# Kernel optimization log

Hardware: AMD Instinct MI355X
Metric: run time of the kernel (lower is better)

## Reference

```python
import jax, jax.numpy as jnp
import numpy as np

IN_CH, H0, H1, OUT_CH = 6, 128, 256, 256
EPS = 1e-5

def _layernorm(x, g, b):
    mu = jnp.mean(x, axis=-1, keepdims=True)
    var = jnp.mean(jnp.square(x - mu), axis=-1, keepdims=True)
    return (x - mu) * jax.lax.rsqrt(var + EPS) * g + b

def setup_inputs() -> dict:
    key = jax.random.key(0)
    ks = jax.random.split(key, 12)
    B, N, C = 8, 65536, 1024
    inp = {
        "point_patches": jax.random.normal(ks[0], (B, N, IN_CH), jnp.float32),
        "nn_idx": jax.random.randint(ks[1], (B, N), 0, C, jnp.int64),
        "center_number": C,
        # conv1: Linear(6,128) -> LN(128) -> GELU -> Linear(128,128)
        "w1": jax.random.normal(ks[2], (IN_CH, H0), jnp.float32) / np.sqrt(IN_CH),
        "b1": jnp.zeros((H0,), jnp.float32),
        "g1": jnp.ones((H0,), jnp.float32),
        "beta1": jnp.zeros((H0,), jnp.float32),
        "w2": jax.random.normal(ks[3], (H0, H0), jnp.float32) / np.sqrt(H0),
        "b2": jnp.zeros((H0,), jnp.float32),
        # conv2: Linear(256,256) -> LN(256) -> GELU -> Linear(256,256)
        "w3": jax.random.normal(ks[4], (2 * H0, H1), jnp.float32) / np.sqrt(2 * H0),
        "b3": jnp.zeros((H1,), jnp.float32),
        "g2": jnp.ones((H1,), jnp.float32),
        "beta2": jnp.zeros((H1,), jnp.float32),
        "w4": jax.random.normal(ks[5], (H1, OUT_CH), jnp.float32) / np.sqrt(H1),
        "b4": jnp.zeros((OUT_CH,), jnp.float32),
    }
    return inp

def _scatter_max_zeros(x, nn_idx, center_number):
    # torch.scatter_reduce(zeros, 1, idx, x, 'max') with include_self=True:
    # segment max clamped from below at 0; empty centers stay 0.
    B = x.shape[0]
    y = jnp.zeros((B, center_number, x.shape[-1]), x.dtype)
    return y.at[jnp.arange(B)[:, None], nn_idx].max(x)

def reference(point_patches, nn_idx, center_number, w1, b1, g1, beta1, w2, b2, w3, b3, g2, beta2, w4, b4):
    # conv1 MLP
    h = point_patches @ w1 + b1
    h = jax.nn.gelu(_layernorm(h, g1, beta1), approximate=False)
    x = h @ w2 + b2                                   # [B, N, H0]
    # scatter-max to centers, gather back per point
    y = _scatter_max_zeros(x, nn_idx, center_number)  # [B, C, H0]
    x_max = jnp.take_along_axis(y, nn_idx[:, :, None], axis=1)  # [B, N, H0]
    x = jnp.concatenate([x_max, x], axis=-1)          # [B, N, 2*H0]
    # conv2 MLP
    h = x @ w3 + b3
    h = jax.nn.gelu(_layernorm(h, g2, beta2), approximate=False)
    x = h @ w4 + b4                                   # [B, N, OUT]
    return _scatter_max_zeros(x, nn_idx, center_number)  # [B, C, OUT]
```

## Files before the change

kernel.cpp:

```cpp
#include <hip/hip_runtime.h>

typedef short short8 __attribute__((ext_vector_type(8)));
typedef float f32x4 __attribute__((ext_vector_type(4)));

#define DEVI __device__ __forceinline__

constexpr int BATCH = 8;
constexpr int NPTS  = 65536;
constexpr int CIN   = 6;
constexpr int H0    = 128;
constexpr int H1    = 256;
constexpr int NCTR  = 1024;
constexpr int MB    = 64;
constexpr int NCHUNK = 8;
constexpr int CHSZ  = NPTS / NCHUNK;

constexpr int A1S = 136;
constexpr int A2S = 264;

constexpr int CAP1 = 8;
constexpr int CAP2 = 4;

constexpr size_t Y_BYTES  = (size_t)BATCH * NCTR * H0 * 4;
constexpr size_t W2T_OFF  = Y_BYTES;
constexpr size_t W3T_OFF  = W2T_OFF + (size_t)H0 * H0 * 2;
constexpr size_t W4T_OFF  = W3T_OFF + (size_t)H1 * H1 * 2;
constexpr size_t SORT_OFF = W4T_OFF + (size_t)H1 * H1 * 2;
constexpr size_t CH_OFF   = SORT_OFF + (size_t)BATCH * NPTS * 4;
constexpr size_t CB_OFF   = CH_OFF + (size_t)BATCH * NCHUNK * NCTR * 4;
constexpr size_t NZR_OFF  = CB_OFF + (size_t)BATCH * NCHUNK * NCTR * 4;
constexpr size_t YQ_OFF   = NZR_OFF + (size_t)BATCH * NCTR * 4;
constexpr size_t WS_NEED  = YQ_OFF + (size_t)BATCH * NCTR * H0 * 2;
constexpr size_t XQ_OFF   = WS_NEED;
constexpr size_t WS_XQ    = XQ_OFF + (size_t)BATCH * NPTS * H0 * 2;

DEVI unsigned short f2bf(float f) {
    unsigned u = __float_as_uint(f);
    u += 0x7fffu + ((u >> 16) & 1u);
    return (unsigned short)(u >> 16);
}
DEVI float gelu(float x) {
    const float x3 = x * x * x;
    const float u = fmaf(x3, -0.07135481283f, -1.5957691216f * x);
    return x * __builtin_amdgcn_rcpf(1.f + __expf(u));
}

DEVI void conv1_tile(int tid, const float* s_pts, const float* s_w1,
                     const float* s_b1, const float* s_g1, const float* s_be1,
                     unsigned short* a1)
{
    const int p = tid >> 2, sub = tid & 3;
    float pt[CIN];
#pragma unroll
    for (int k = 0; k < CIN; ++k) pt[k] = s_pts[p * CIN + k];
    float h[32];
#pragma unroll
    for (int j = 0; j < 32; ++j) {
        const int c = (j << 2) + sub;
        float a = s_b1[c];
#pragma unroll
        for (int k = 0; k < CIN; ++k) a = fmaf(pt[k], s_w1[k * H0 + c], a);
        h[j] = a;
    }
    float s = 0.f, s2 = 0.f;
#pragma unroll
    for (int j = 0; j < 32; ++j) { s += h[j]; s2 = fmaf(h[j], h[j], s2); }
    s  += __shfl_xor(s, 1);  s  += __shfl_xor(s, 2);
    s2 += __shfl_xor(s2, 1); s2 += __shfl_xor(s2, 2);
    const float mean = s * (1.f / H0);
    const float rstd = rsqrtf(s2 * (1.f / H0) - mean * mean + 1e-5f);
#pragma unroll
    for (int j = 0; j < 32; ++j) {
        const int c = (j << 2) + sub;
        float v = fmaf((h[j] - mean) * rstd, s_g1[c], s_be1[c]);
        a1[p * A1S + c] = f2bf(gelu(v));
    }
}

DEVI void gemm2(int lane, int wave, const unsigned short* a1,
                const unsigned short* __restrict__ w2T, f32x4 (&acc)[4][2])
{
    const int q = lane >> 4, colw = lane & 15, n0 = wave * 32;
#pragma unroll
    for (int ks = 0; ks < 4; ++ks) {
        short8 af[4], bfr[2];
#pragma unroll
        for (int mt = 0; mt < 4; ++mt)
            af[mt] = *(const short8*)&a1[(mt * 16 + colw) * A1S + ks * 32 + q * 8];
#pragma unroll
        for (int nt = 0; nt < 2; ++nt)
            bfr[nt] = *(const short8*)&w2T[(n0 + nt * 16 + colw) * H0 + ks * 32 + q * 8];
#pragma unroll
        for (int mt = 0; mt < 4; ++mt)
#pragma unroll
            for (int nt = 0; nt < 2; ++nt)
                acc[mt][nt] = __builtin_amdgcn_mfma_f32_16x16x32_bf16(
                    af[mt], bfr[nt], acc[mt][nt], 0, 0, 0);
    }
}

DEVI void stage_sorted(int tid, int b, int P0, const int* __restrict__ sorted,
                       const float* __restrict__ pts, float* s_pts, int* s_idx)
{
    if (tid < 64) {
        const int val = sorted[P0 + tid];
        const int pid = val & 0xFFFF;
        s_idx[tid] = (val >> 16) & (NCTR - 1);
        const float* prow = &pts[((size_t)(b << 16) + pid) * CIN];
#pragma unroll
        for (int k = 0; k < CIN; ++k) s_pts[tid * CIN + k] = prow[k];
    }
}

DEVI void slot_scan(int tid, const int* s_idx, int* s_slot, int* s_slotc, int* s_nslot, int cap)
{
    int f = 0;
    if (tid < MB) {
        f = (tid > 0 && s_idx[tid] != s_idx[tid - 1]) ? 1 : 0;
        s_slot[tid] = f;
    }
    __syncthreads();
#pragma unroll
    for (int off = 1; off < MB; off <<= 1) {
        int t = 0;
        if (tid < MB && tid >= off) t = s_slot[tid - off];
        __syncthreads();
        if (tid < MB) s_slot[tid] += t;
        __syncthreads();
    }
    if (tid < MB) {
        const int s = s_slot[tid];
        if ((f || tid == 0) && s < cap) s_slotc[s] = s_idx[tid];
        if (tid == MB - 1) *s_nslot = (s + 1 < cap) ? (s + 1) : cap;
    }
    __syncthreads();
}

__global__ __launch_bounds__(256) void k_prep(
    const float* __restrict__ w2, const float* __restrict__ w3,
    const float* __restrict__ w4,
    unsigned short* __restrict__ w2T, unsigned short* __restrict__ w3T,
    unsigned short* __restrict__ w4T)
{
    int t = blockIdx.x * 256 + threadIdx.x;
    if (t < H0 * H0) {
        int n = t >> 7, k = t & 127;
        w2T[t] = f2bf(w2[k * H0 + n]);
    }
    int t3 = t - H0 * H0;
    if (t3 >= 0 && t3 < H1 * H1) {
        int n = t3 >> 8, k = t3 & 255;
        w3T[t3] = f2bf(w3[k * H1 + n]);
    }
    int t4 = t - (H0 * H0 + H1 * H1);
    if (t4 >= 0 && t4 < H1 * H1) {
        int n = t4 >> 8, k = t4 & 255;
        w4T[t4] = f2bf(w4[k * H1 + n]);
    }
}

__global__ __launch_bounds__(256) void k_yq(const float* __restrict__ y,
                                            unsigned short* __restrict__ yq)
{
    const int i = blockIdx.x * 256 + threadIdx.x;
    const float4 v = *(const float4*)&y[(size_t)i * 4];
    uint2 pk;
    pk.x = (unsigned)f2bf(v.x) | ((unsigned)f2bf(v.y) << 16);
    pk.y = (unsigned)f2bf(v.z) | ((unsigned)f2bf(v.w) << 16);
    *(uint2*)&yq[(size_t)i * 4] = pk;
}

__global__ __launch_bounds__(256) void k_hist(const int* __restrict__ nn,
                                              int* __restrict__ ch)
{
    __shared__ int lh[NCTR];
    const int tid = threadIdx.x;
    const int b = blockIdx.x >> 3, k = blockIdx.x & 7;
    const int base = (b << 16) + k * CHSZ;
    for (int c = tid; c < NCTR; c += 256) lh[c] = 0;
    __syncthreads();
    for (int i = tid; i < CHSZ; i += 256)
        atomicAdd(&lh[nn[base + i] & (NCTR - 1)], 1);
    __syncthreads();
    for (int c = tid; c < NCTR; c += 256) ch[(blockIdx.x << 10) + c] = lh[c];
}

__global__ __launch_bounds__(256) void k_scan(const int* __restrict__ ch,
                                              int* __restrict__ cb,
                                              int* __restrict__ nzr)
{
    __shared__ int part[256], partz[256];
    const int tid = threadIdx.x;
    const int b = tid >> 5, t = tid & 31;
    const int c0 = t * 32;
    int tot = 0, totz = 0;
    for (int c = c0; c < c0 + 32; ++c) {
        int cnt = 0;
        for (int k = 0; k < NCHUNK; ++k)
            cnt += ch[((b * NCHUNK + k) << 10) + c];
        tot += cnt; totz += (cnt > 0);
    }
    part[tid] = tot; partz[tid] = totz;
    __syncthreads();
    if (t == 0) {
        int run = 0, runz = 0;
        for (int i = 0; i < 32; ++i) {
            const int v  = part[(b << 5) + i];  part[(b << 5) + i]  = run;  run  += v;
            const int vz = partz[(b << 5) + i]; partz[(b << 5) + i] = runz; runz += vz;
        }
    }
    __syncthreads();
    int run = part[tid], runz = partz[tid];
    for (int c = c0; c < c0 + 32; ++c) {
        int cnt = 0;
        for (int k = 0; k < NCHUNK; ++k) {
            const int idx = ((b * NCHUNK + k) << 10) + c;
            cb[idx] = run; run += ch[idx]; cnt += ch[idx];
        }
        nzr[(b << 10) + c] = runz;
        runz += (cnt > 0);
    }
}

__global__ __launch_bounds__(256) void k_scatter(const int* __restrict__ nn,
                                                 const int* __restrict__ cb,
                                                 int* __restrict__ sorted)
{
    __shared__ int cur[NCTR];
    const int tid = threadIdx.x;
    const int b = blockIdx.x >> 3, k = blockIdx.x & 7;
    const int base = (b << 16) + k * CHSZ;
    for (int c = tid; c < NCTR; c += 256) cur[c] = cb[(blockIdx.x << 10) + c];
    __syncthreads();
    for (int i = tid; i < CHSZ; i += 256) {
        const int c = nn[base + i] & (NCTR - 1);
        const int pos = atomicAdd(&cur[c], 1);
        if ((unsigned)pos < (unsigned)NPTS)
            sorted[(b << 16) + pos] = (k * CHSZ + i) | (c << 16);
    }
}

template <bool XQ>
__global__ __launch_bounds__(256, 4) void k_phase1(
    const int* __restrict__ sorted, const float* __restrict__ pts,
    const int* __restrict__ nzr,
    const float* __restrict__ w1, const float* __restrict__ b1,
    const float* __restrict__ g1, const float* __restrict__ be1,
    const unsigned short* __restrict__ w2T, const float* __restrict__ b2,
    float* __restrict__ y, unsigned short* __restrict__ xq)
{
    __shared__ __align__(16) float s_pts[MB * CIN];
    __shared__ int   s_idx[MB], s_slot[MB], s_slotc[CAP1], s_nslot;
    __shared__ float s_w1[CIN * H0];
    __shared__ float s_b1[H0], s_g1[H0], s_be1[H0];
    __shared__ __align__(16) unsigned short a1[MB * A1S];
    __shared__ int   red1[CAP1 * H0];

    const int tid = threadIdx.x;
    const int P0  = blockIdx.x * MB;
    const int b   = P0 >> 16;
    const int lane = tid & 63, wave = tid >> 6;
    const int q = lane >> 4, colw = lane & 15, n0 = wave * 32;

    if (tid < 64) {
        const int val = sorted[P0 + tid];
        const int pid = val & 0xFFFF;
        const int c   = (val >> 16) & (NCTR - 1);
        const int c0v = (sorted[P0] >> 16) & (NCTR - 1);
        s_idx[tid] = c;
        const int sl = nzr[(b << 10) + c] - nzr[(b << 10) + c0v];
        s_slot[tid] = sl;
        if (tid == 63) s_nslot = (sl + 1 < CAP1) ? (sl + 1) : CAP1;
        const float* prow = &pts[((size_t)(b << 16) + pid) * CIN];
#pragma unroll
        for (int k = 0; k < CIN; ++k) s_pts[tid * CIN + k] = prow[k];
    }
    for (int i = tid; i < CIN * H0; i += 256) s_w1[i] = w1[i];
    if (tid < H0) { s_b1[tid] = b1[tid]; s_g1[tid] = g1[tid]; s_be1[tid] = be1[tid]; }
    for (int i = tid; i < CAP1 * H0; i += 256) red1[i] = 0;
    __syncthreads();

    if (tid < 64) {
        const int sl = s_slot[tid];
        if (sl < CAP1 && (tid == 0 || s_idx[tid] != s_idx[tid - 1]))
            s_slotc[sl] = s_idx[tid];
    }
    conv1_tile(tid, s_pts, s_w1, s_b1, s_g1, s_be1, a1);
    __syncthreads();

    f32x4 acc[4][2] = {};
    gemm2(lane, wave, a1, w2T, acc);
    if (XQ) __syncthreads();

    float b2reg[2];
#pragma unroll
    for (int nt = 0; nt < 2; ++nt) b2reg[nt] = b2[n0 + nt * 16 + colw];

    int* yi = (int*)y;
    {
        float vm[2] = {-3.4e38f, -3.4e38f};
        int cur = s_slot[q * 4], curc = s_idx[q * 4];
#pragma unroll
        for (int mt = 0; mt < 4; ++mt)
#pragma unroll
            for (int r = 0; r < 4; ++r) {
                const int row = mt * 16 + q * 4 + r;
                const int s = s_slot[row];
                if (s != cur) {
#pragma unroll
                    for (int nt = 0; nt < 2; ++nt) {
                        if (vm[nt] > 0.f) {
                            const int col = n0 + nt * 16 + colw;
                            if (cur < CAP1) atomicMax(&red1[cur * H0 + col], __float_as_int(vm[nt]));
                            else atomicMax(&yi[(((b << 10) + curc) << 7) + col], __float_as_int(vm[nt]));
                        }
                        vm[nt] = -3.4e38f;
                    }
                    cur = s; curc = s_idx[row];
                }
#pragma unroll
                for (int nt = 0; nt < 2; ++nt) {
                    const float v = acc[mt][nt][r] + b2reg[nt];
                    if (XQ) a1[row * A1S + n0 + nt * 16 + colw] = f2bf(v);
                    vm[nt] = fmaxf(vm[nt], v);
                }
            }
#pragma unroll
        for (int nt = 0; nt < 2; ++nt)
            if (vm[nt] > 0.f) {
                const int col = n0 + nt * 16 + colw;
                if (cur < CAP1) atomicMax(&red1[cur * H0 + col], __float_as_int(vm[nt]));
                else atomicMax(&yi[(((b << 10) + curc) << 7) + col], __float_as_int(vm[nt]));
            }
    }
    __syncthreads();
    const int nsc = s_nslot;
    for (int i = tid; i < nsc * H0; i += 256) {
        const int v = red1[i];
        if (v > 0)
            atomicMax(&yi[(((b << 10) + s_slotc[i >> 7]) << 7) + (i & 127)], v);
    }
    if (XQ) {
        for (int i = tid; i < MB * (H0 / 8); i += 256) {
            const int row = i >> 4, u = (i & 15) * 8;
            *(short8*)&xq[((size_t)P0 + row) * H0 + u] = *(const short8*)&a1[row * A1S + u];
        }
    }
}

__global__ __launch_bounds__(512, 6) void k_phase2x(
    const int* __restrict__ sorted, const unsigned short* __restrict__ xq,
    const unsigned short* __restrict__ yq, const int* __restrict__ nzr,
    const unsigned short* __restrict__ w3T, const float* __restrict__ b3,
    const float* __restrict__ g2, const float* __restrict__ be2,
    const unsigned short* __restrict__ w4T, const float* __restrict__ b4,
    float* __restrict__ outp)
{
    __shared__ int   s_idx[MB], s_slot[MB], s_slotc[CAP2], s_nslot;
    __shared__ __align__(16) unsigned short a2[MB * A2S];
    __shared__ union __align__(16) {
        float2 stats[MB * 8];
        int    red[CAP2 * H1];
    } u2;
    __shared__ float2 s_rowstat[MB];

    const int tid = threadIdx.x;
    const int P0  = blockIdx.x * MB;
    const int b   = P0 >> 16;
    const int lane = tid & 63, wave = tid >> 6;
    const int q = lane >> 4, colw = lane & 15;
    const int n0 = wave * 32;

    const int rowp = tid >> 3, sub = tid & 7;
    {
        const int sval = sorted[P0 + rowp];
        const int cp = (sval >> 16) & (NCTR - 1);
        const unsigned short* src;
        unsigned short* dst;
        if (sub < 4) {
            src = &yq[((size_t)((b << 10) + cp)) * H0 + sub * 32];
            dst = &a2[rowp * A2S + sub * 32];
        } else {
            src = &xq[((size_t)P0 + rowp) * H0 + (sub - 4) * 32];
            dst = &a2[rowp * A2S + H0 + (sub - 4) * 32];
        }
#pragma unroll
        for (int u = 0; u < 4; ++u)
            *(short8*)(dst + u * 8) = *(const short8*)(src + u * 8);
    }
    if (tid < 64) {
        const int c   = (sorted[P0 + tid] >> 16) & (NCTR - 1);
        const int c0v = (sorted[P0] >> 16) & (NCTR - 1);
        s_idx[tid] = c;
        const int sl = nzr[(b << 10) + c] - nzr[(b << 10) + c0v];
        s_slot[tid] = sl;
        if (tid == 63) s_nslot = (sl + 1 < CAP2) ? (sl + 1) : CAP2;
    }
    __syncthreads();

    if (tid < 64) {
        const int sl = s_slot[tid];
        if (sl < CAP2 && (tid == 0 || s_idx[tid] != s_idx[tid - 1]))
            s_slotc[sl] = s_idx[tid];
    }

    f32x4 acc3[4][2] = {};
#pragma unroll
    for (int ks = 0; ks < 8; ++ks) {
        short8 af[4], bfr[2];
#pragma unroll
        for (int mt = 0; mt < 4; ++mt)
            af[mt] = *(const short8*)&a2[(mt * 16 + colw) * A2S + ks * 32 + q * 8];
#pragma unroll
        for (int nt = 0; nt < 2; ++nt)
            bfr[nt] = *(const short8*)&w3T[(n0 + nt * 16 + colw) * H1 + ks * 32 + q * 8];
#pragma unroll
        for (int mt = 0; mt < 4; ++mt)
#pragma unroll
            for (int nt = 0; nt < 2; ++nt)
                acc3[mt][nt] = __builtin_amdgcn_mfma_f32_16x16x32_bf16(
                    af[mt], bfr[nt], acc3[mt][nt], 0, 0, 0);
    }

    {
        float b3r[2];
#pragma unroll
        for (int nt = 0; nt < 2; ++nt) b3r[nt] = b3[n0 + nt * 16 + colw];
#pragma unroll
        for (int mt = 0; mt < 4; ++mt)
#pragma unroll
            for (int nt = 0; nt < 2; ++nt)
#pragma unroll
                for (int r = 0; r < 4; ++r)
                    acc3[mt][nt][r] += b3r[nt];
    }

#pragma unroll
    for (int mt = 0; mt < 4; ++mt)
#pragma unroll
        for (int r = 0; r < 4; ++r) {
            float s = 0.f, s2 = 0.f;
#pragma unroll
            for (int nt = 0; nt < 2; ++nt) {
                float v = acc3[mt][nt][r];
                s += v; s2 = fmaf(v, v, s2);
            }
            s  += __shfl_xor(s, 1);  s  += __shfl_xor(s, 2);
            s  += __shfl_xor(s, 4);  s  += __shfl_xor(s, 8);
            s2 += __shfl_xor(s2, 1); s2 += __shfl_xor(s2, 2);
            s2 += __shfl_xor(s2, 4); s2 += __shfl_xor(s2, 8);
            if (colw == 0)
                u2.stats[(mt * 16 + q * 4 + r) * 8 + wave] = make_float2(s, s2);
        }
    __syncthreads();
    if (tid < MB) {
        float S = 0.f, S2 = 0.f;
#pragma unroll
        for (int w = 0; w < 8; ++w) { float2 t = u2.stats[tid * 8 + w]; S += t.x; S2 += t.y; }
        const float mean = S * (1.f / H1);
        const float rstd = rsqrtf(S2 * (1.f / H1) - mean * mean + 1e-5f);
        s_rowstat[tid] = make_float2(mean, rstd);
    }
    __syncthreads();

    {
        float g2r[2], be2r[2];
#pragma unroll
        for (int nt = 0; nt < 2; ++nt) {
            const int col = n0 + nt * 16 + colw;
            g2r[nt] = g2[col]; be2r[nt] = be2[col];
        }
#pragma unroll
        for (int mt = 0; mt < 4; ++mt)
#pragma unroll
            for (int r = 0; r < 4; ++r) {
                const int row = mt * 16 + q * 4 + r;
                const float2 ms = s_rowstat[row];
#pragma unroll
                for (int nt = 0; nt < 2; ++nt) {
                    float v = (acc3[mt][nt][r] - ms.x) * ms.y;
                    v = fmaf(v, g2r[nt], be2r[nt]);
                    a2[row * A2S + n0 + nt * 16 + colw] = f2bf(gelu(v));
                }
            }
    }
    for (int i = tid; i < CAP2 * H1; i += 512) u2.red[i] = 0;
    __syncthreads();

    f32x4 acc4[4][2] = {};
#pragma unroll
    for (int ks = 0; ks < 8; ++ks) {
        short8 af[4], bfr[2];
#pragma unroll
        for (int mt = 0; mt < 4; ++mt)
            af[mt] = *(const short8*)&a2[(mt * 16 + colw) * A2S + ks * 32 + q * 8];
#pragma unroll
        for (int nt = 0; nt < 2; ++nt)
            bfr[nt] = *(const short8*)&w4T[(n0 + nt * 16 + colw) * H1 + ks * 32 + q * 8];
#pragma unroll
        for (int mt = 0; mt < 4; ++mt)
#pragma unroll
            for (int nt = 0; nt < 2; ++nt)
                acc4[mt][nt] = __builtin_amdgcn_mfma_f32_16x16x32_bf16(
                    af[mt], bfr[nt], acc4[mt][nt], 0, 0, 0);
    }

    float b4r[2];
#pragma unroll
    for (int nt = 0; nt < 2; ++nt) b4r[nt] = b4[n0 + nt * 16 + colw];

    int* outi = (int*)outp;
    {
        float vm[2] = {-3.4e38f, -3.4e38f};
        int cur = s_slot[q * 4], curc = s_idx[q * 4];
#pragma unroll
        for (int mt = 0; mt < 4; ++mt)
#pragma unroll
            for (int r = 0; r < 4; ++r) {
                const int row = mt * 16 + q * 4 + r;
                const int s = s_slot[row];
                if (s != cur) {
#pragma unroll
                    for (int nt = 0; nt < 2; ++nt) {
                        if (vm[nt] > 0.f) {
                            const int col = n0 + nt * 16 + colw;
                            if (cur < CAP2) atomicMax(&u2.red[cur * H1 + col], __float_as_int(vm[nt]));
                            else atomicMax(&outi[(((size_t)(b << 10) + curc) << 8) + col], __float_as_int(vm[nt]));
                        }
                        vm[nt] = -3.4e38f;
                    }
                    cur = s; curc = s_idx[row];
                }
#pragma unroll
                for (int nt = 0; nt < 2; ++nt)
                    vm[nt] = fmaxf(vm[nt], acc4[mt][nt][r] + b4r[nt]);
            }
#pragma unroll
        for (int nt = 0; nt < 2; ++nt)
            if (vm[nt] > 0.f) {
                const int col = n0 + nt * 16 + colw;
                if (cur < CAP2) atomicMax(&u2.red[cur * H1 + col], __float_as_int(vm[nt]));
                else atomicMax(&outi[(((size_t)(b << 10) + curc) << 8) + col], __float_as_int(vm[nt]));
            }
    }
    __syncthreads();
    const int nsc = s_nslot;
    for (int i = tid; i < nsc * H1; i += 512) {
        const int v = u2.red[i];
        if (v > 0)
            atomicMax(&outi[(((size_t)(b << 10) + s_slotc[i >> 8]) << 8) + (i & 255)], v);
    }
}

__global__ __launch_bounds__(256) void k_phase2r(
    const int* __restrict__ sorted, const float* __restrict__ pts,
    const float* __restrict__ w1, const float* __restrict__ b1,
    const float* __restrict__ g1, const float* __restrict__ be1,
    const unsigned short* __restrict__ w2T, const float* __restrict__ b2,
    const float* __restrict__ y,
    const unsigned short* __restrict__ w3T, const float* __restrict__ b3,
    const float* __restrict__ g2, const float* __restrict__ be2,
    const unsigned short* __restrict__ w4T, const float* __restrict__ b4,
    float* __restrict__ outp)
{
    __shared__ __align__(16) float s_pts[MB * CIN];
    __shared__ int   s_idx[MB], s_slot[MB], s_slotc[CAP2], s_nslot;
    __shared__ float s_w1[CIN * H0];
    __shared__ float s_b1[H0], s_g1[H0], s_be1[H0], s_b2[H0];
    __shared__ float s_b3[H1], s_g2[H1], s_be2[H1], s_b4[H1];
    __shared__ union __align__(16) {
        unsigned short a1[MB * A1S];
        struct { float2 stats[MB * 4]; float2 rowstat[MB]; } ln;
        int red[CAP2 * H1];
    } u1;
    __shared__ __align__(16) unsigned short a2[MB * A2S];

    const int tid = threadIdx.x;
    const int P0  = blockIdx.x * MB;
    const int b   = P0 >> 16;

    stage_sorted(tid, b, P0, sorted, pts, s_pts, s_idx);
    for (int i = tid; i < CIN * H0; i += 256) s_w1[i] = w1[i];
    if (tid < H0) { s_b1[tid] = b1[tid]; s_g1[tid] = g1[tid]; s_be1[tid] = be1[tid]; s_b2[tid] = b2[tid]; }
    if (tid < H1) { s_b3[tid] = b3[tid]; s_g2[tid] = g2[tid]; s_be2[tid] = be2[tid]; s_b4[tid] = b4[tid]; }
    __syncthreads();

    conv1_tile(tid, s_pts, s_w1, s_b1, s_g1, s_be1, u1.a1);
    slot_scan(tid, s_idx, s_slot, s_slotc, &s_nslot, CAP2);

    f32x4 acc2[4][2] = {};
    const int lane = tid & 63, wave = tid >> 6;
    gemm2(lane, wave, u1.a1, w2T, acc2);

    const int q = lane >> 4, colw = lane & 15;
    {
        const int n0 = wave * 32;
#pragma unroll
        for (int mt = 0; mt < 4; ++mt)
#pragma unroll
            for (int nt = 0; nt < 2; ++nt)
#pragma unroll
                for (int r = 0; r < 4; ++r) {
                    const int row = mt * 16 + q * 4 + r;
                    const int col = n0 + nt * 16 + colw;
                    a2[row * A2S + H0 + col] = f2bf(acc2[mt][nt][r] + s_b2[col]);
                }
    }
    {
        const int p = tid >> 2, sub = tid & 3;
        const float* yrow = y + ((size_t)((b << 10) + s_idx[p])) * H0;
#pragma unroll
        for (int j4 = 0; j4 < 8; ++j4) {
            const int c = sub * 32 + j4 * 4;
            float4 v = *(const float4*)&yrow[c];
            uint2 pk;
            pk.x = (unsigned)f2bf(v.x) | ((unsigned)f2bf(v.y) << 16);
            pk.y = (unsigned)f2bf(v.z) | ((unsigned)f2bf(v.w) << 16);
            *(uint2*)&a2[p * A2S + c] = pk;
        }
    }
    __syncthreads();

    f32x4 acc3[4][4] = {};
    const int n0 = wave * 64;
#pragma unroll
    for (int ks = 0; ks < 8; ++ks) {
        short8 af[4], bfr[4];
#pragma unroll
        for (int mt = 0; mt < 4; ++mt)
            af[mt] = *(const short8*)&a2[(mt * 16 + colw) * A2S + ks * 32 + q * 8];
#pragma unroll
        for (int nt = 0; nt < 4; ++nt)
            bfr[nt] = *(const short8*)&w3T[(n0 + nt * 16 + colw) * H1 + ks * 32 + q * 8];
#pragma unroll
        for (int mt = 0; mt < 4; ++mt)
#pragma unroll
            for (int nt = 0; nt < 4; ++nt)
                acc3[mt][nt] = __builtin_amdgcn_mfma_f32_16x16x32_bf16(
                    af[mt], bfr[nt], acc3[mt][nt], 0, 0, 0);
    }

#pragma unroll
    for (int mt = 0; mt < 4; ++mt)
#pragma unroll
        for (int nt = 0; nt < 4; ++nt)
#pragma unroll
            for (int r = 0; r < 4; ++r)
                acc3[mt][nt][r] += s_b3[n0 + nt * 16 + colw];

#pragma unroll
    for (int mt = 0; mt < 4; ++mt)
#pragma unroll
        for (int r = 0; r < 4; ++r) {
            float s = 0.f, s2 = 0.f;
#pragma unroll
            for (int nt = 0; nt < 4; ++nt) {
                float v = acc3[mt][nt][r];
                s += v; s2 = fmaf(v, v, s2);
            }
            s  += __shfl_xor(s, 1);  s  += __shfl_xor(s, 2);
            s  += __shfl_xor(s, 4);  s  += __shfl_xor(s, 8);
            s2 += __shfl_xor(s2, 1); s2 += __shfl_xor(s2, 2);
            s2 += __shfl_xor(s2, 4); s2 += __shfl_xor(s2, 8);
            if (colw == 0)
                u1.ln.stats[(mt * 16 + q * 4 + r) * 4 + wave] = make_float2(s, s2);
        }
    __syncthreads();
    if (tid < MB) {
        float S = 0.f, S2 = 0.f;
#pragma unroll
        for (int w = 0; w < 4; ++w) { float2 t = u1.ln.stats[tid * 4 + w]; S += t.x; S2 += t.y; }
        const float mean = S * (1.f / H1);
        const float rstd = rsqrtf(S2 * (1.f / H1) - mean * mean + 1e-5f);
        u1.ln.rowstat[tid] = make_float2(mean, rstd);
    }
    __syncthreads();

#pragma unroll
    for (int mt = 0; mt < 4; ++mt)
#pragma unroll
        for (int r = 0; r < 4; ++r) {
            const int row = mt * 16 + q * 4 + r;
            const float2 ms = u1.ln.rowstat[row];
#pragma unroll
            for (int nt = 0; nt < 4; ++nt) {
                const int col = n0 + nt * 16 + colw;
                float v = (acc3[mt][nt][r] - ms.x) * ms.y;
                v = fmaf(v, s_g2[col], s_be2[col]);
                a2[row * A2S + col] = f2bf(gelu(v));
            }
        }
    __syncthreads();

    for (int i = tid; i < CAP2 * H1; i += 256) u1.red[i] = 0;

    f32x4 acc4[4][4] = {};
#pragma unroll
    for (int ks = 0; ks < 8; ++ks) {
        short8 af[4], bfr[4];
#pragma unroll
        for (int mt = 0; mt < 4; ++mt)
            af[mt] = *(const short8*)&a2[(mt * 16 + colw) * A2S + ks * 32 + q * 8];
#pragma unroll
        for (int nt = 0; nt < 4; ++nt)
            bfr[nt] = *(const short8*)&w4T[(n0 + nt * 16 + colw) * H1 + ks * 32 + q * 8];
#pragma unroll
        for (int mt = 0; mt < 4; ++mt)
#pragma unroll
            for (int nt = 0; nt < 4; ++nt)
                acc4[mt][nt] = __builtin_amdgcn_mfma_f32_16x16x32_bf16(
                    af[mt], bfr[nt], acc4[mt][nt], 0, 0, 0);
    }
    __syncthreads();

    int* outi = (int*)outp;
#pragma unroll
    for (int mt = 0; mt < 4; ++mt)
#pragma unroll
        for (int nt = 0; nt < 4; ++nt)
#pragma unroll
            for (int r = 0; r < 4; ++r) {
                const int row = mt * 16 + q * 4 + r;
                const int col = n0 + nt * 16 + colw;
                const float v = acc4[mt][nt][r] + s_b4[col];
                if (v > 0.f) {
                    const int s = s_slot[row];
                    if (s < CAP2)
                        atomicMax(&u1.red[s * H1 + col], __float_as_int(v));
                    else
                        atomicMax(&outi[(((size_t)(b << 10) + s_idx[row]) << 8) + col],
                                  __float_as_int(v));
                }
            }
    __syncthreads();
    const int nsc = s_nslot;
    for (int i = tid; i < nsc * H1; i += 256) {
        const int v = u1.red[i];
        if (v > 0)
            atomicMax(&outi[(((size_t)(b << 10) + s_slotc[i >> 8]) << 8) + (i & 255)], v);
    }
}

extern "C" void kernel_launch(void* const* d_in, const int* in_sizes, int n_in,
                              void* d_out, int out_size, void* d_ws, size_t ws_size,
                              hipStream_t stream)
{
    const float* pts = (const float*)d_in[0];
    const int*   nn  = (const int*)d_in[1];
    const float* w1  = (const float*)d_in[3];
    const float* b1  = (const float*)d_in[4];
    const float* g1  = (const float*)d_in[5];
    const float* be1 = (const float*)d_in[6];
    const float* w2  = (const float*)d_in[7];
    const float* b2  = (const float*)d_in[8];
    const float* w3  = (const float*)d_in[9];
    const float* b3  = (const float*)d_in[10];
    const float* g2  = (const float*)d_in[11];
    const float* be2 = (const float*)d_in[12];
    const float* w4  = (const float*)d_in[13];
    const float* b4  = (const float*)d_in[14];

    if (ws_size < WS_NEED) return;

    char* ws = (char*)d_ws;
    float*          y      = (float*)(ws);
    unsigned short* w2T    = (unsigned short*)(ws + W2T_OFF);
    unsigned short* w3T    = (unsigned short*)(ws + W3T_OFF);
    unsigned short* w4T    = (unsigned short*)(ws + W4T_OFF);
    int*            sorted = (int*)(ws + SORT_OFF);
    int*            ch     = (int*)(ws + CH_OFF);
    int*            cb     = (int*)(ws + CB_OFF);
    int*            nzr    = (int*)(ws + NZR_OFF);
    unsigned short* yq     = (unsigned short*)(ws + YQ_OFF);
    unsigned short* xq     = (unsigned short*)(ws + XQ_OFF);
    float* outp = (float*)d_out;
    const bool have_xq = ws_size >= WS_XQ;

    hipMemsetAsync(y, 0, Y_BYTES, stream);
    hipMemsetAsync(outp, 0, (size_t)out_size * sizeof(float), stream);

    k_prep<<<576, 256, 0, stream>>>(w2, w3, w4, w2T, w3T, w4T);
    k_hist<<<BATCH * NCHUNK, 256, 0, stream>>>(nn, ch);
    k_scan<<<1, 256, 0, stream>>>(ch, cb, nzr);
    k_scatter<<<BATCH * NCHUNK, 256, 0, stream>>>(nn, cb, sorted);

    const int nblk = BATCH * NPTS / MB;
    if (have_xq) {
        k_phase1<true><<<nblk, 256, 0, stream>>>(sorted, pts, nzr, w1, b1, g1, be1, w2T, b2, y, xq);
        k_yq<<<BATCH * NCTR * H0 / 4 / 256, 256, 0, stream>>>(y, yq);
        k_phase2x<<<nblk, 512, 0, stream>>>(sorted, xq, yq, nzr, w3T, b3, g2, be2, w4T, b4, outp);
    } else {
        k_phase1<false><<<nblk, 256, 0, stream>>>(sorted, pts, nzr, w1, b1, g1, be1, w2T, b2, y, nullptr);
        k_phase2r<<<nblk, 256, 0, stream>>>(sorted, pts, w1, b1, g1, be1, w2T, b2, y,
                                            w3T, b3, g2, be2, w4T, b4, outp);
    }
}
```

Measured before the change: 441.6 us.

## Make phase2x persistent over four tiles with register prefetch of next tile

The phase-2 kernel now processes four 64-point tiles per block in a grid-strided loop, launching a quarter as many blocks. While the current tile is computed, it loads the next tile's gathered yq/xq rows into registers so global latency overlaps with MFMA work. This amortizes block launch and prologue cost, at the price of extra registers (which may lower occupancy under launch bounds 512,6) and an added barrier per tile.

Measured after the change: 966.5 us. +118.9%, slower.

```diff
diff --git a/kernel.cpp b/kernel.cpp
--- a/kernel.cpp
+++ b/kernel.cpp
@@ -14,6 +14,8 @@
 constexpr int MB    = 64;
 constexpr int NCHUNK = 8;
 constexpr int CHSZ  = NPTS / NCHUNK;
+constexpr int NTILE = 4;
+constexpr int P2GRID = BATCH * NPTS / MB / NTILE;
 
 constexpr int A1S = 136;
 constexpr int A2S = 264;
@@ -365,190 +367,214 @@
     __shared__ float2 s_rowstat[MB];
 
     const int tid = threadIdx.x;
-    const int P0  = blockIdx.x * MB;
-    const int b   = P0 >> 16;
     const int lane = tid & 63, wave = tid >> 6;
     const int q = lane >> 4, colw = lane & 15;
     const int n0 = wave * 32;
-
     const int rowp = tid >> 3, sub = tid & 7;
+    int* outi = (int*)outp;
+
+    int P0 = blockIdx.x * MB;
+    short8 sv0, sv1, sv2, sv3;
     {
         const int sval = sorted[P0 + rowp];
         const int cp = (sval >> 16) & (NCTR - 1);
-        const unsigned short* src;
-        unsigned short* dst;
-        if (sub < 4) {
-            src = &yq[((size_t)((b << 10) + cp)) * H0 + sub * 32];
-            dst = &a2[rowp * A2S + sub * 32];
-        } else {
-            src = &xq[((size_t)P0 + rowp) * H0 + (sub - 4) * 32];
-            dst = &a2[rowp * A2S + H0 + (sub - 4) * 32];
-        }
-#pragma unroll
-        for (int u = 0; u < 4; ++u)
-            *(short8*)(dst + u * 8) = *(const short8*)(src + u * 8);
-    }
-    if (tid < 64) {
-        const int c   = (sorted[P0 + tid] >> 16) & (NCTR - 1);
-        const int c0v = (sorted[P0] >> 16) & (NCTR - 1);
-        s_idx[tid] = c;
-        const int sl = nzr[(b << 10) + c] - nzr[(b << 10) + c0v];
-        s_slot[tid] = sl;
-        if (tid == 63) s_nslot = (sl + 1 < CAP2) ? (sl + 1) : CAP2;
-    }
-    __syncthreads();
-
-    if (tid < 64) {
-        const int sl = s_slot[tid];
-        if (sl < CAP2 && (tid == 0 || s_idx[tid] != s_idx[tid - 1]))
-            s_slotc[sl] = s_idx[tid];
-    }
-
-    f32x4 acc3[4][2] = {};
-#pragma unroll
-    for (int ks = 0; ks < 8; ++ks) {
-        short8 af[4], bfr[2];
+        const int b0 = P0 >> 16;
+        const unsigned short* src = (sub < 4)
+            ? &yq[((size_t)((b0 << 10) + cp)) * H0 + sub * 32]
+            : &xq[((size_t)P0 + rowp) * H0 + (sub - 4) * 32];
+        sv0 = *(const short8*)(src);
+        sv1 = *(const short8*)(src + 8);
+        sv2 = *(const short8*)(src + 16);
+        sv3 = *(const short8*)(src + 24);
+    }
+
+    for (int t = 0; t < NTILE; ++t) {
+        const int b = P0 >> 16;
+        {
+            unsigned short* dst = (sub < 4)
+                ? &a2[rowp * A2S + sub * 32]
+                : &a2[rowp * A2S + H0 + (sub - 4) * 32];
+            *(short8*)(dst)      = sv0;
+            *(short8*)(dst + 8)  = sv1;
+            *(short8*)(dst + 16) = sv2;
+            *(short8*)(dst + 24) = sv3;
+        }
+        if (tid < 64) {
+            const int c   = (sorted[P0 + tid] >> 16) & (NCTR - 1);
+            const int c0v = (sorted[P0] >> 16) & (NCTR - 1);
+            s_idx[tid] = c;
+            const int sl = nzr[(b << 10) + c] - nzr[(b << 10) + c0v];
+            s_slot[tid] = sl;
+            if (tid == 63) s_nslot = (sl + 1 < CAP2) ? (sl + 1) : CAP2;
+        }
+        __syncthreads();
+
+        const int P0n = P0 + P2GRID * MB;
+        if (t + 1 < NTILE) {
+            const int svaln = sorted[P0n + rowp];
+            const int cpn = (svaln >> 16) & (NCTR - 1);
+            const int bn = P0n >> 16;
+            const unsigned short* srcn = (sub < 4)
+                ? &yq[((size_t)((bn << 10) + cpn)) * H0 + sub * 32]
+                : &xq[((size_t)P0n + rowp) * H0 + (sub - 4) * 32];
+            sv0 = *(const short8*)(srcn);
+            sv1 = *(const short8*)(srcn + 8);
+            sv2 = *(const short8*)(srcn + 16);
+            sv3 = *(const short8*)(srcn + 24);
+        }
+        if (tid < 64) {
+            const int sl = s_slot[tid];
+            if (sl < CAP2 && (tid == 0 || s_idx[tid] != s_idx[tid - 1]))
+                s_slotc[sl] = s_idx[tid];
+        }
+
+        f32x4 acc3[4][2] = {};
+#pragma unroll
+        for (int ks = 0; ks < 8; ++ks) {
+            short8 af[4], bfr[2];
+#pragma unroll
+            for (int mt = 0; mt < 4; ++mt)
+                af[mt] = *(const short8*)&a2[(mt * 16 + colw) * A2S + ks * 32 + q * 8];
+#pragma unroll
+            for (int nt = 0; nt < 2; ++nt)
+                bfr[nt] = *(const short8*)&w3T[(n0 + nt * 16 + colw) * H1 + ks * 32 + q * 8];
+#pragma unroll
+            for (int mt = 0; mt < 4; ++mt)
+#pragma unroll
+                for (int nt = 0; nt < 2; ++nt)
+                    acc3[mt][nt] = __builtin_amdgcn_mfma_f32_16x16x32_bf16(
+                        af[mt], bfr[nt], acc3[mt][nt], 0, 0, 0);
+        }
+
+        {
+            float b3r[2];
+#pragma unroll
+            for (int nt = 0; nt < 2; ++nt) b3r[nt] = b3[n0 + nt * 16 + colw];
+#pragma unroll
+            for (int mt = 0; mt < 4; ++mt)
+#pragma unroll
+                for (int nt = 0; nt < 2; ++nt)
+#pragma unroll
+                    for (int r = 0; r < 4; ++r)
+                        acc3[mt][nt][r] += b3r[nt];
+        }
+
 #pragma unroll
         for (int mt = 0; mt < 4; ++mt)
-            af[mt] = *(const short8*)&a2[(mt * 16 + colw) * A2S + ks * 32 + q * 8];
-#pragma unroll
-        for (int nt = 0; nt < 2; ++nt)
-            bfr[nt] = *(const short8*)&w3T[(n0 + nt * 16 + colw) * H1 + ks * 32 + q * 8];
-#pragma unroll
-        for (int mt = 0; mt < 4; ++mt)
+#pragma unroll
+            for (int r = 0; r < 4; ++r) {
+                float s = 0.f, s2 = 0.f;
+#pragma unroll
+                for (int nt = 0; nt < 2; ++nt) {
+                    float v = acc3[mt][nt][r];
+                    s += v; s2 = fmaf(v, v, s2);
+                }
+                s  += __shfl_xor(s, 1);  s  += __shfl_xor(s, 2);
+                s  += __shfl_xor(s, 4);  s  += __shfl_xor(s, 8);
+                s2 += __shfl_xor(s2, 1); s2 += __shfl_xor(s2, 2);
+                s2 += __shfl_xor(s2, 4); s2 += __shfl_xor(s2, 8);
+                if (colw == 0)
+                    u2.stats[(mt * 16 + q * 4 + r) * 8 + wave] = make_float2(s, s2);
+            }
+        __syncthreads();
+        if (tid < MB) {
+            float S = 0.f, S2 = 0.f;
+#pragma unroll
+            for (int w = 0; w < 8; ++w) { float2 tt = u2.stats[tid * 8 + w]; S += tt.x; S2 += tt.y; }
+            const float mean = S * (1.f / H1);
+            const float rstd = rsqrtf(S2 * (1.f / H1) - mean * mean + 1e-5f);
+            s_rowstat[tid] = make_float2(mean, rstd);
+        }
+        __syncthreads();
+
+        {
+            float g2r[2], be2r[2];
+#pragma unroll
+            for (int nt = 0; nt < 2; ++nt) {
+                const int col = n0 + nt * 16 + colw;
+                g2r[nt] = g2[col]; be2r[nt] = be2[col];
+            }
+#pragma unroll
+            for (int mt = 0; mt < 4; ++mt)
+#pragma unroll
+                for (int r = 0; r < 4; ++r) {
+                    const int row = mt * 16 + q * 4 + r;
+                    const float2 ms = s_rowstat[row];
+#pragma unroll
+                    for (int nt = 0; nt < 2; ++nt) {
+                        float v = (acc3[mt][nt][r] - ms.x) * ms.y;
+                        v = fmaf(v, g2r[nt], be2r[nt]);
+                        a2[row * A2S + n0 + nt * 16 + colw] = f2bf(gelu(v));
+                    }
+                }
+        }
+        for (int i = tid; i < CAP2 * H1; i += 512) u2.red[i] = 0;
+        __syncthreads();
+
+        f32x4 acc4[4][2] = {};
+#pragma unroll
+        for (int ks = 0; ks < 8; ++ks) {
+            short8 af[4], bfr[2];
+#pragma unroll
+            for (int mt = 0; mt < 4; ++mt)
+                af[mt] = *(const short8*)&a2[(mt * 16 + colw) * A2S + ks * 32 + q * 8];
 #pragma unroll
             for (int nt = 0; nt < 2; ++nt)
-                acc3[mt][nt] = __builtin_amdgcn_mfma_f32_16x16x32_bf16(
-                    af[mt], bfr[nt], acc3[mt][nt], 0, 0, 0);
-    }
-
-    {
-        float b3r[2];
-#pragma unroll
-        for (int nt = 0; nt < 2; ++nt) b3r[nt] = b3[n0 + nt * 16 + colw];
-#pragma unroll
-        for (int mt = 0; mt < 4; ++mt)
+                bfr[nt] = *(const short8*)&w4T[(n0 + nt * 16 + colw) * H1 + ks * 32 + q * 8];
+#pragma unroll
+            for (int mt = 0; mt < 4; ++mt)
+#pragma unroll
+                for (int nt = 0; nt < 2; ++nt)
+                    acc4[mt][nt] = __builtin_amdgcn_mfma_f32_16x16x32_bf16(
+                        af[mt], bfr[nt], acc4[mt][nt], 0, 0, 0);
+        }
+
+        float b4r[2];
+#pragma unroll
+        for (int nt = 0; nt < 2; ++nt) b4r[nt] = b4[n0 + nt * 16 + colw];
+
+        {
+            float vm[2] = {-3.4e38f, -3.4e38f};
+            int cur = s_slot[q * 4], curc = s_idx[q * 4];
+#pragma unroll
+            for (int mt = 0; mt < 4; ++mt)
+#pragma unroll
+                for (int r = 0; r < 4; ++r) {
+                    const int row = mt * 16 + q * 4 + r;
+                    const int s = s_slot[row];
+                    if (s != cur) {
+#pragma unroll
+                        for (int nt = 0; nt < 2; ++nt) {
+                            if (vm[nt] > 0.f) {
+                                const int col = n0 + nt * 16 + colw;
+                                if (cur < CAP2) atomicMax(&u2.red[cur * H1 + col], __float_as_int(vm[nt]));
+                                else atomicMax(&outi[(((size_t)(b << 10) + curc) << 8) + col], __float_as_int(vm[nt]));
+                            }
+                            vm[nt] = -3.4e38f;
+                        }
+                        cur = s; curc = s_idx[row];
+                    }
+#pragma unroll
+                    for (int nt = 0; nt < 2; ++nt)
+                        vm[nt] = fmaxf(vm[nt], acc4[mt][nt][r] + b4r[nt]);
+                }
 #pragma unroll
             for (int nt = 0; nt < 2; ++nt)
-#pragma unroll
-                for (int r = 0; r < 4; ++r)
-                    acc3[mt][nt][r] += b3r[nt];
-    }
-
-#pragma unroll
-    for (int mt = 0; mt < 4; ++mt)
-#pragma unroll
-        for (int r = 0; r < 4; ++r) {
-            float s = 0.f, s2 = 0.f;
-#pragma unroll
-            for (int nt = 0; nt < 2; ++nt) {
-                float v = acc3[mt][nt][r];
-                s += v; s2 = fmaf(v, v, s2);
-            }
-            s  += __shfl_xor(s, 1);  s  += __shfl_xor(s, 2);
-            s  += __shfl_xor(s, 4);  s  += __shfl_xor(s, 8);
-            s2 += __shfl_xor(s2, 1); s2 += __shfl_xor(s2, 2);
-            s2 += __shfl_xor(s2, 4); s2 += __shfl_xor(s2, 8);
-            if (colw == 0)
-                u2.stats[(mt * 16 + q * 4 + r) * 8 + wave] = make_float2(s, s2);
-        }
-    __syncthreads();
-    if (tid < MB) {
-        float S = 0.f, S2 = 0.f;
-#pragma unroll
-        for (int w = 0; w < 8; ++w) { float2 t = u2.stats[tid * 8 + w]; S += t.x; S2 += t.y; }
-        const float mean = S * (1.f / H1);
-        const float rstd = rsqrtf(S2 * (1.f / H1) - mean * mean + 1e-5f);
-        s_rowstat[tid] = make_float2(mean, rstd);
-    }
-    __syncthreads();
-
-    {
-        float g2r[2], be2r[2];
-#pragma unroll
-        for (int nt = 0; nt < 2; ++nt) {
-            const int col = n0 + nt * 16 + colw;
-            g2r[nt] = g2[col]; be2r[nt] = be2[col];
-        }
-#pragma unroll
-        for (int mt = 0; mt < 4; ++mt)
-#pragma unroll
-            for (int r = 0; r < 4; ++r) {
-                const int row = mt * 16 + q * 4 + r;
-                const float2 ms = s_rowstat[row];
-#pragma unroll
-                for (int nt = 0; nt < 2; ++nt) {
-                    float v = (acc3[mt][nt][r] - ms.x) * ms.y;
-                    v = fmaf(v, g2r[nt], be2r[nt]);
-                    a2[row * A2S + n0 + nt * 16 + colw] = f2bf(gelu(v));
+                if (vm[nt] > 0.f) {
+                    const int col = n0 + nt * 16 + colw;
+                    if (cur < CAP2) atomicMax(&u2.red[cur * H1 + col], __float_as_int(vm[nt]));
+                    else atomicMax(&outi[(((size_t)(b << 10) + curc) << 8) + col], __float_as_int(vm[nt]));
                 }
-            }
-    }
-    for (int i = tid; i < CAP2 * H1; i += 512) u2.red[i] = 0;
-    __syncthreads();
-
-    f32x4 acc4[4][2] = {};
-#pragma unroll
-    for (int ks = 0; ks < 8; ++ks) {
-        short8 af[4], bfr[2];
-#pragma unroll
-        for (int mt = 0; mt < 4; ++mt)
-            af[mt] = *(const short8*)&a2[(mt * 16 + colw) * A2S + ks * 32 + q * 8];
-#pragma unroll
-        for (int nt = 0; nt < 2; ++nt)
-            bfr[nt] = *(const short8*)&w4T[(n0 + nt * 16 + colw) * H1 + ks * 32 + q * 8];
-#pragma unroll
-        for (int mt = 0; mt < 4; ++mt)
-#pragma unroll
-            for (int nt = 0; nt < 2; ++nt)
-                acc4[mt][nt] = __builtin_amdgcn_mfma_f32_16x16x32_bf16(
-                    af[mt], bfr[nt], acc4[mt][nt], 0, 0, 0);
-    }
-
-    float b4r[2];
-#pragma unroll
-    for (int nt = 0; nt < 2; ++nt) b4r[nt] = b4[n0 + nt * 16 + colw];
-
-    int* outi = (int*)outp;
-    {
-        float vm[2] = {-3.4e38f, -3.4e38f};
-        int cur = s_slot[q * 4], curc = s_idx[q * 4];
-#pragma unroll
-        for (int mt = 0; mt < 4; ++mt)
-#pragma unroll
-            for (int r = 0; r < 4; ++r) {
-                const int row = mt * 16 + q * 4 + r;
-                const int s = s_slot[row];
-                if (s != cur) {
-#pragma unroll
-                    for (int nt = 0; nt < 2; ++nt) {
-                        if (vm[nt] > 0.f) {
-                            const int col = n0 + nt * 16 + colw;
-                            if (cur < CAP2) atomicMax(&u2.red[cur * H1 + col], __float_as_int(vm[nt]));
-                            else atomicMax(&outi[(((size_t)(b << 10) + curc) << 8) + col], __float_as_int(vm[nt]));
-                        }
-                        vm[nt] = -3.4e38f;
-                    }
-                    cur = s; curc = s_idx[row];
-                }
-#pragma unroll
-                for (int nt = 0; nt < 2; ++nt)
-                    vm[nt] = fmaxf(vm[nt], acc4[mt][nt][r] + b4r[nt]);
-            }
-#pragma unroll
-        for (int nt = 0; nt < 2; ++nt)
-            if (vm[nt] > 0.f) {
-                const int col = n0 + nt * 16 + colw;
-                if (cur < CAP2) atomicMax(&u2.red[cur * H1 + col], __float_as_int(vm[nt]));
-                else atomicMax(&outi[(((size_t)(b << 10) + curc) << 8) + col], __float_as_int(vm[nt]));
-            }
-    }
-    __syncthreads();
-    const int nsc = s_nslot;
-    for (int i = tid; i < nsc * H1; i += 512) {
-        const int v = u2.red[i];
-        if (v > 0)
-            atomicMax(&outi[(((size_t)(b << 10) + s_slotc[i >> 8]) << 8) + (i & 255)], v);
+        }
+        __syncthreads();
+        const int nsc = s_nslot;
+        for (int i = tid; i < nsc * H1; i += 512) {
+            const int v = u2.red[i];
+            if (v > 0)
+                atomicMax(&outi[(((size_t)(b << 10) + s_slotc[i >> 8]) << 8) + (i & 255)], v);
+        }
+        __syncthreads();
+        P0 = P0n;
     }
 }
 
@@ -788,7 +814,7 @@
     if (have_xq) {
         k_phase1<true><<<nblk, 256, 0, stream>>>(sorted, pts, nzr, w1, b1, g1, be1, w2T, b2, y, xq);
         k_yq<<<BATCH * NCTR * H0 / 4 / 256, 256, 0, stream>>>(y, yq);
-        k_phase2x<<<nblk, 512, 0, stream>>>(sorted, xq, yq, nzr, w3T, b3, g2, be2, w4T, b4, outp);
+        k_phase2x<<<P2GRID, 512, 0, stream>>>(sorted, xq, yq, nzr, w3T, b3, g2, be2, w4T, b4, outp);
     } else {
         k_phase1<false><<<nblk, 256, 0, stream>>>(sorted, pts, nzr, w1, b1, g1, be1, w2T, b2, y, nullptr);
         k_phase2r<<<nblk, 256, 0, stream>>>(sorted, pts, w1, b1, g1, be1, w2T, b2, y,
```
